# Optimization experiments

Measured on AMD Instinct MI355X. Metric: run time of the kernel, lower is better.

Reference implementation:

```python
import jax, jax.numpy as jnp
import numpy as np

B, N, D = 8192, 49, 3
D3 = 42  # embed_dim // 3
E = 128
K = 3    # min(3, N-1) nearest neighbors for local density


def setup_inputs() -> dict:
    key = jax.random.key(0)
    ks = jax.random.split(key, 8)
    points = jax.random.normal(ks[0], (B, N, D), jnp.float32)
    return {
        "points": points,
        "W_dist": jax.random.normal(ks[1], (1, D3), jnp.float32) * 1.0,
        "b_dist": jnp.zeros((D3,), jnp.float32),
        "emb": jax.random.normal(ks[2], (50, D3), jnp.float32) * 0.02,
        "W_den": jax.random.normal(ks[3], (1, D3), jnp.float32) * 1.0,
        "b_den": jnp.zeros((D3,), jnp.float32),
        "W_out": jax.random.normal(ks[4], (3 * D3, E), jnp.float32) * (1.0 / np.sqrt(3 * D3)),
        "b_out": jnp.zeros((E,), jnp.float32),
    }


def _local_density(points):
    # Batched cdist with diagonal masked to +inf, then mean of K smallest dists.
    sq = jnp.sum(points * points, axis=-1)                      # [B,N]
    d2 = sq[:, :, None] + sq[:, None, :] \
         - 2.0 * jnp.einsum('bnd,bmd->bnm', points, points)      # [B,N,N]
    d2 = jnp.maximum(d2, 0.0)
    eye = jnp.eye(points.shape[1], dtype=bool)
    d2 = jnp.where(eye, jnp.inf, d2)
    dists = jnp.sqrt(d2)
    nearest = -jax.lax.top_k(-dists, K)[0]                      # [B,N,K] smallest
    return jnp.mean(nearest, axis=-1, keepdims=True)            # [B,N,1]


def reference(points, W_dist, b_dist, emb, W_den, b_den, W_out, b_out):
    b, n, _ = points.shape
    centroid = jnp.mean(points, axis=1, keepdims=True)          # [B,1,3]
    rel = points - centroid
    centroid_dist = jnp.linalg.norm(rel, axis=-1, keepdims=True)  # [B,N,1]
    dist_f = centroid_dist @ W_dist + b_dist                    # [B,N,D3]
    # n_valid == N (no mask), a constant index into the count embedding
    count_f = jnp.broadcast_to(emb[n][None, None, :], (b, n, emb.shape[1]))
    density = _local_density(points)                            # [B,N,1]
    den_f = density @ W_den + b_den                             # [B,N,D3]
    features = jnp.concatenate([dist_f, count_f, den_f], axis=-1)  # [B,N,3*D3]
    return features @ W_out + b_out                             # [B,N,E]
```

## Files before the change

kernel.cpp:

```cpp
#include <hip/hip_runtime.h>
#include <math.h>

#define N_     49
#define D3_    42
#define E_     128
#define WPB    4


__global__ __launch_bounds__(256) void fused_all(
        const float* __restrict__ points,
        const float* __restrict__ W_dist,
        const float* __restrict__ b_dist,
        const float* __restrict__ emb,
        const float* __restrict__ W_den,
        const float* __restrict__ b_den,
        const float* __restrict__ W_out,
        const float* __restrict__ b_out,
        float4* __restrict__ out4,
        int B) {
    __shared__ float4 pts4[WPB][N_];
    __shared__ __align__(16) float sUVC[3 * E_];

    const int tid  = threadIdx.x;
    const int lane = tid & 63;
    const int w    = tid >> 6;
    const int wid  = blockIdx.x * WPB + w;
    const bool v0  = (wid < B);

    const int n = (lane < N_) ? lane : N_ - 1;
    float px = 0.f, py = 0.f, pz = 0.f;
    if (v0) {
        const float* pb = points + (long long)wid * (N_ * 3) + 3 * n;
        px = pb[0]; py = pb[1]; pz = pb[2];
    }

    if (tid < E_) {
        const float* embN = emb + N_ * D3_;
        float u = 0.f, vv = 0.f, c = b_out[tid];
        for (int j = 0; j < D3_; ++j) {
            float w0 = W_out[j * E_ + tid];
            float w1 = W_out[(D3_ + j) * E_ + tid];
            float w2 = W_out[(2 * D3_ + j) * E_ + tid];
            u  = fmaf(W_dist[j], w0, u);
            vv = fmaf(W_den[j],  w2, vv);
            c  = fmaf(b_dist[j], w0, c);
            c  = fmaf(embN[j],   w1, c);
            c  = fmaf(b_den[j],  w2, c);
        }
        sUVC[tid]          = u;
        sUVC[E_ + tid]     = vv;
        sUVC[2 * E_ + tid] = c;
    }

    if (v0 && lane < N_) {
        pts4[w][lane] = make_float4(px, py, pz, 0.f);
    }

    float cd = 0.f, dn = 0.f;
    if (v0) {
        float sx = 0.f, sy = 0.f, sz = 0.f;
        float t0 = INFINITY, t1 = INFINITY, t2 = INFINITY;
        for (int m = 0; m < N_; ++m) {
            float4 qq = pts4[w][m];
            sx += qq.x; sy += qq.y; sz += qq.z;
            float dx = px - qq.x, dy = py - qq.y, dz = pz - qq.z;
            float d2 = fmaf(dx, dx, fmaf(dy, dy, dz * dz));
            if (m != n) {
                if (d2 < t0)      { t2 = t1; t1 = t0; t0 = d2; }
                else if (d2 < t1) { t2 = t1; t1 = d2; }
                else if (d2 < t2) { t2 = d2; }
            }
        }
        const float inv = 1.0f / (float)N_;
        float cx = sx * inv, cy = sy * inv, cz = sz * inv;
        float ex = px - cx, ey = py - cy, ez = pz - cz;
        cd = sqrtf(fmaf(ex, ex, fmaf(ey, ey, ez * ez)));
        dn = (sqrtf(t0) + sqrtf(t1) + sqrtf(t2)) * (1.0f / 3.0f);
    }

    __syncthreads();
    const int q = lane & 31;
    const float4 u4 = *(const float4*)&sUVC[4 * q];
    const float4 v4 = *(const float4*)&sUVC[E_ + 4 * q];
    const float4 c4 = *(const float4*)&sUVC[2 * E_ + 4 * q];

    if (v0) {
        float4* ob = out4 + (long long)wid * (N_ * 32);
#pragma unroll
        for (int j = 0; j < 25; ++j) {
            int row = 2 * j + (lane >> 5);
            float a = __shfl(cd, row);
            float d = __shfl(dn, row);
            if (row < N_) {
                float4 r;
                r.x = fmaf(a, u4.x, fmaf(d, v4.x, c4.x));
                r.y = fmaf(a, u4.y, fmaf(d, v4.y, c4.y));
                r.z = fmaf(a, u4.z, fmaf(d, v4.z, c4.z));
                r.w = fmaf(a, u4.w, fmaf(d, v4.w, c4.w));
                ob[row * 32 + q] = r;
            }
        }
    }
}

extern "C" void kernel_launch(void* const* d_in, const int* in_sizes, int n_in,
                              void* d_out, int out_size, void* d_ws, size_t ws_size,
                              hipStream_t stream) {
    const float* points = (const float*)d_in[0];
    const float* W_dist = (const float*)d_in[1];
    const float* b_dist = (const float*)d_in[2];
    const float* emb    = (const float*)d_in[3];
    const float* W_den  = (const float*)d_in[4];
    const float* b_den  = (const float*)d_in[5];
    const float* W_out  = (const float*)d_in[6];
    const float* b_out  = (const float*)d_in[7];

    const int B = in_sizes[0] / (N_ * 3);
    const int nblocks = (B + WPB - 1) / WPB;

    fused_all<<<nblocks, 64 * WPB, 0, stream>>>(
        points, W_dist, b_dist, emb, W_den, b_den, W_out, b_out,
        (float4*)d_out, B);
}
```

Baseline: 227.2 us.

## Precompute UVC projection in a setup kernel and use nontemporal output stores

Moves the per-block folding of W_out with the distance, count and density weights into a one-block setup kernel that writes 384 floats to workspace. The main kernel then loads them directly from global memory and drops the block-wide barrier, so every block no longer repeats the 42-step weight reduction. Output stores become nontemporal to avoid cache pollution on the large streaming write. The cost is an extra kernel launch and a dependency on the workspace being large enough, with the old in-block path kept as a fallback.

```diff
diff --git a/kernel.cpp b/kernel.cpp
--- a/kernel.cpp
+++ b/kernel.cpp
@@ -6,7 +6,37 @@
 #define E_     128
 #define WPB    4
 
+typedef float f32x4 __attribute__((ext_vector_type(4)));
 
+
+__global__ __launch_bounds__(128) void uvc_setup(
+        const float* __restrict__ W_dist,
+        const float* __restrict__ b_dist,
+        const float* __restrict__ emb,
+        const float* __restrict__ W_den,
+        const float* __restrict__ b_den,
+        const float* __restrict__ W_out,
+        const float* __restrict__ b_out,
+        float* __restrict__ uvc) {
+    const int tid = threadIdx.x;
+    const float* embN = emb + N_ * D3_;
+    float u = 0.f, vv = 0.f, c = b_out[tid];
+    for (int j = 0; j < D3_; ++j) {
+        float w0 = W_out[j * E_ + tid];
+        float w1 = W_out[(D3_ + j) * E_ + tid];
+        float w2 = W_out[(2 * D3_ + j) * E_ + tid];
+        u  = fmaf(W_dist[j], w0, u);
+        vv = fmaf(W_den[j],  w2, vv);
+        c  = fmaf(b_dist[j], w0, c);
+        c  = fmaf(embN[j],   w1, c);
+        c  = fmaf(b_den[j],  w2, c);
+    }
+    uvc[tid]          = u;
+    uvc[E_ + tid]     = vv;
+    uvc[2 * E_ + tid] = c;
+}
+
+template <bool USE_WS>
 __global__ __launch_bounds__(256) void fused_all(
         const float* __restrict__ points,
         const float* __restrict__ W_dist,
@@ -16,7 +46,8 @@
         const float* __restrict__ b_den,
         const float* __restrict__ W_out,
         const float* __restrict__ b_out,
-        float4* __restrict__ out4,
+        const float* __restrict__ uvc,
+        f32x4* __restrict__ out4,
         int B) {
     __shared__ float4 pts4[WPB][N_];
     __shared__ __align__(16) float sUVC[3 * E_];
@@ -26,6 +57,7 @@
     const int w    = tid >> 6;
     const int wid  = blockIdx.x * WPB + w;
     const bool v0  = (wid < B);
+    const int q    = lane & 31;
 
     const int n = (lane < N_) ? lane : N_ - 1;
     float px = 0.f, py = 0.f, pz = 0.f;
@@ -34,22 +66,29 @@
         px = pb[0]; py = pb[1]; pz = pb[2];
     }
 
-    if (tid < E_) {
-        const float* embN = emb + N_ * D3_;
-        float u = 0.f, vv = 0.f, c = b_out[tid];
-        for (int j = 0; j < D3_; ++j) {
-            float w0 = W_out[j * E_ + tid];
-            float w1 = W_out[(D3_ + j) * E_ + tid];
-            float w2 = W_out[(2 * D3_ + j) * E_ + tid];
-            u  = fmaf(W_dist[j], w0, u);
-            vv = fmaf(W_den[j],  w2, vv);
-            c  = fmaf(b_dist[j], w0, c);
-            c  = fmaf(embN[j],   w1, c);
-            c  = fmaf(b_den[j],  w2, c);
+    f32x4 u4, v4, c4;
+    if (USE_WS) {
+        u4 = *(const f32x4*)&uvc[4 * q];
+        v4 = *(const f32x4*)&uvc[E_ + 4 * q];
+        c4 = *(const f32x4*)&uvc[2 * E_ + 4 * q];
+    } else {
+        if (tid < E_) {
+            const float* embN = emb + N_ * D3_;
+            float u = 0.f, vv = 0.f, c = b_out[tid];
+            for (int j = 0; j < D3_; ++j) {
+                float w0 = W_out[j * E_ + tid];
+                float w1 = W_out[(D3_ + j) * E_ + tid];
+                float w2 = W_out[(2 * D3_ + j) * E_ + tid];
+                u  = fmaf(W_dist[j], w0, u);
+                vv = fmaf(W_den[j],  w2, vv);
+                c  = fmaf(b_dist[j], w0, c);
+                c  = fmaf(embN[j],   w1, c);
+                c  = fmaf(b_den[j],  w2, c);
+            }
+            sUVC[tid]          = u;
+            sUVC[E_ + tid]     = vv;
+            sUVC[2 * E_ + tid] = c;
         }
-        sUVC[tid]          = u;
-        sUVC[E_ + tid]     = vv;
-        sUVC[2 * E_ + tid] = c;
     }
 
     if (v0 && lane < N_) {
@@ -78,26 +117,27 @@
         dn = (sqrtf(t0) + sqrtf(t1) + sqrtf(t2)) * (1.0f / 3.0f);
     }
 
-    __syncthreads();
-    const int q = lane & 31;
-    const float4 u4 = *(const float4*)&sUVC[4 * q];
-    const float4 v4 = *(const float4*)&sUVC[E_ + 4 * q];
-    const float4 c4 = *(const float4*)&sUVC[2 * E_ + 4 * q];
+    if (!USE_WS) {
+        __syncthreads();
+        u4 = *(const f32x4*)&sUVC[4 * q];
+        v4 = *(const f32x4*)&sUVC[E_ + 4 * q];
+        c4 = *(const f32x4*)&sUVC[2 * E_ + 4 * q];
+    }
 
     if (v0) {
-        float4* ob = out4 + (long long)wid * (N_ * 32);
+        f32x4* ob = out4 + (long long)wid * (N_ * 32);
 #pragma unroll
         for (int j = 0; j < 25; ++j) {
             int row = 2 * j + (lane >> 5);
             float a = __shfl(cd, row);
             float d = __shfl(dn, row);
             if (row < N_) {
-                float4 r;
+                f32x4 r;
                 r.x = fmaf(a, u4.x, fmaf(d, v4.x, c4.x));
                 r.y = fmaf(a, u4.y, fmaf(d, v4.y, c4.y));
                 r.z = fmaf(a, u4.z, fmaf(d, v4.z, c4.z));
                 r.w = fmaf(a, u4.w, fmaf(d, v4.w, c4.w));
-                ob[row * 32 + q] = r;
+                __builtin_nontemporal_store(r, &ob[row * 32 + q]);
             }
         }
     }
@@ -118,7 +158,16 @@
     const int B = in_sizes[0] / (N_ * 3);
     const int nblocks = (B + WPB - 1) / WPB;
 
-    fused_all<<<nblocks, 64 * WPB, 0, stream>>>(
-        points, W_dist, b_dist, emb, W_den, b_den, W_out, b_out,
-        (float4*)d_out, B);
+    if (ws_size >= 3 * E_ * sizeof(float)) {
+        float* uvc = (float*)d_ws;
+        uvc_setup<<<1, E_, 0, stream>>>(
+            W_dist, b_dist, emb, W_den, b_den, W_out, b_out, uvc);
+        fused_all<true><<<nblocks, 64 * WPB, 0, stream>>>(
+            points, W_dist, b_dist, emb, W_den, b_den, W_out, b_out,
+            uvc, (f32x4*)d_out, B);
+    } else {
+        fused_all<false><<<nblocks, 64 * WPB, 0, stream>>>(
+            points, W_dist, b_dist, emb, W_den, b_den, W_out, b_out,
+            (const float*)nullptr, (f32x4*)d_out, B);
+    }
 }
```

Result: slower. 239.8 us (+5.5%).

## Split into precompute kernel and grid-stride nontemporal output streaming kernel

Applied to the files above, without the earlier changes.

Splits the fused kernel in two. The first kernel computes the per-point centroid distance and local density, plus the folded weight vectors (computed only in block 0), and writes them to workspace. The second is a grid-stride kernel that writes the large output with nontemporal stores, aiming for better store bandwidth and less cache pollution. In exchange it adds a second launch and a workspace round trip, and it falls back to the fused kernel when the workspace is too small.

```diff
diff --git a/kernel.cpp b/kernel.cpp
--- a/kernel.cpp
+++ b/kernel.cpp
@@ -6,6 +6,105 @@
 #define E_     128
 #define WPB    4
 
+typedef float f32x4 __attribute__((ext_vector_type(4)));
+
+
+__global__ __launch_bounds__(256) void precomp(
+        const float* __restrict__ points,
+        const float* __restrict__ W_dist,
+        const float* __restrict__ b_dist,
+        const float* __restrict__ emb,
+        const float* __restrict__ W_den,
+        const float* __restrict__ b_den,
+        const float* __restrict__ W_out,
+        const float* __restrict__ b_out,
+        float* __restrict__ ws,
+        int B) {
+    __shared__ float4 pts4[WPB][N_];
+
+    const int tid  = threadIdx.x;
+    const int lane = tid & 63;
+    const int w    = tid >> 6;
+    const int wid  = blockIdx.x * WPB + w;
+    const bool v0  = (wid < B);
+
+    const int n = (lane < N_) ? lane : N_ - 1;
+    float px = 0.f, py = 0.f, pz = 0.f;
+    if (v0) {
+        const float* pb = points + (long long)wid * (N_ * 3) + 3 * n;
+        px = pb[0]; py = pb[1]; pz = pb[2];
+    }
+
+    if (blockIdx.x == 0 && tid < E_) {
+        const float* embN = emb + N_ * D3_;
+        float u = 0.f, vv = 0.f, c = b_out[tid];
+        for (int j = 0; j < D3_; ++j) {
+            float w0 = W_out[j * E_ + tid];
+            float w1 = W_out[(D3_ + j) * E_ + tid];
+            float w2 = W_out[(2 * D3_ + j) * E_ + tid];
+            u  = fmaf(W_dist[j], w0, u);
+            vv = fmaf(W_den[j],  w2, vv);
+            c  = fmaf(b_dist[j], w0, c);
+            c  = fmaf(embN[j],   w1, c);
+            c  = fmaf(b_den[j],  w2, c);
+        }
+        ws[tid]          = u;
+        ws[E_ + tid]     = vv;
+        ws[2 * E_ + tid] = c;
+    }
+
+    if (!v0) return;
+
+    if (lane < N_) pts4[w][lane] = make_float4(px, py, pz, 0.f);
+
+    float sx = 0.f, sy = 0.f, sz = 0.f;
+    float t0 = INFINITY, t1 = INFINITY, t2 = INFINITY;
+    for (int m = 0; m < N_; ++m) {
+        float4 qq = pts4[w][m];
+        sx += qq.x; sy += qq.y; sz += qq.z;
+        float dx = px - qq.x, dy = py - qq.y, dz = pz - qq.z;
+        float d2 = fmaf(dx, dx, fmaf(dy, dy, dz * dz));
+        if (m != n) {
+            if (d2 < t0)      { t2 = t1; t1 = t0; t0 = d2; }
+            else if (d2 < t1) { t2 = t1; t1 = d2; }
+            else if (d2 < t2) { t2 = d2; }
+        }
+    }
+    const float inv = 1.0f / (float)N_;
+    float cx = sx * inv, cy = sy * inv, cz = sz * inv;
+    float ex = px - cx, ey = py - cy, ez = pz - cz;
+    float cd = sqrtf(fmaf(ex, ex, fmaf(ey, ey, ez * ez)));
+    float dn = (sqrtf(t0) + sqrtf(t1) + sqrtf(t2)) * (1.0f / 3.0f);
+
+    if (lane < N_) {
+        float2* cddn = (float2*)(ws + 3 * E_);
+        cddn[wid * N_ + lane] = make_float2(cd, dn);
+    }
+}
+
+__global__ __launch_bounds__(256) void stream_out(
+        const float* __restrict__ ws,
+        f32x4* __restrict__ out4,
+        int M) {
+    const int g = blockIdx.x * 256 + threadIdx.x;
+    const int q = g & 31;
+    const f32x4 u4 = *(const f32x4*)&ws[4 * q];
+    const f32x4 v4 = *(const f32x4*)&ws[E_ + 4 * q];
+    const f32x4 c4 = *(const f32x4*)&ws[2 * E_ + 4 * q];
+    const float2* __restrict__ cddn = (const float2*)(ws + 3 * E_);
+    const int stride = gridDim.x * 256;
+
+#pragma unroll 4
+    for (int i = g; i < M; i += stride) {
+        float2 t = cddn[i >> 5];
+        f32x4 r;
+        r.x = fmaf(t.x, u4.x, fmaf(t.y, v4.x, c4.x));
+        r.y = fmaf(t.x, u4.y, fmaf(t.y, v4.y, c4.y));
+        r.z = fmaf(t.x, u4.z, fmaf(t.y, v4.z, c4.z));
+        r.w = fmaf(t.x, u4.w, fmaf(t.y, v4.w, c4.w));
+        __builtin_nontemporal_store(r, &out4[i]);
+    }
+}
 
 __global__ __launch_bounds__(256) void fused_all(
         const float* __restrict__ points,
@@ -52,9 +151,7 @@
         sUVC[2 * E_ + tid] = c;
     }
 
-    if (v0 && lane < N_) {
-        pts4[w][lane] = make_float4(px, py, pz, 0.f);
-    }
+    if (v0 && lane < N_) pts4[w][lane] = make_float4(px, py, pz, 0.f);
 
     float cd = 0.f, dn = 0.f;
     if (v0) {
@@ -116,9 +213,19 @@
     const float* b_out  = (const float*)d_in[7];
 
     const int B = in_sizes[0] / (N_ * 3);
-    const int nblocks = (B + WPB - 1) / WPB;
-
-    fused_all<<<nblocks, 64 * WPB, 0, stream>>>(
-        points, W_dist, b_dist, emb, W_den, b_den, W_out, b_out,
-        (float4*)d_out, B);
-}
+    const size_t ws_needed = (size_t)(3 * E_) * 4 + (size_t)B * N_ * 8;
+
+    if (ws_size >= ws_needed) {
+        float* ws = (float*)d_ws;
+        const int nblk_a = (B + WPB - 1) / WPB;
+        precomp<<<nblk_a, 64 * WPB, 0, stream>>>(
+            points, W_dist, b_dist, emb, W_den, b_den, W_out, b_out, ws, B);
+        const int M = B * N_ * 32;
+        stream_out<<<2048, 256, 0, stream>>>(ws, (f32x4*)d_out, M);
+    } else {
+        const int nblocks = (B + WPB - 1) / WPB;
+        fused_all<<<nblocks, 64 * WPB, 0, stream>>>(
+            points, W_dist, b_dist, emb, W_den, b_den, W_out, b_out,
+            (float4*)d_out, B);
+    }
+}
```

After: 239.3 us. +5.3%, slower.
